# Kernel tuning notes

Hardware: AMD Instinct MI355X
Metric: run time of the kernel (lower is better)

The kernel has to match this reference:

```python
import jax, jax.numpy as jnp
import numpy as np

B, N, M, D, NHEAD, FF, C, K = 2, 16384, 2048, 256, 8, 512, 50, 3
HID = 128          # embed/pos hidden
HEAD_HID = 256     # seg head hidden
L = 4              # depth
EPS = 1e-5


def setup_inputs() -> dict:
    key = jax.random.key(0)
    ks = jax.random.split(key, 32)
    g = lambda i, shape: jax.random.normal(ks[i], shape, dtype=jnp.float32) * 0.02
    z = lambda shape: jnp.zeros(shape, jnp.float32)
    o = lambda shape: jnp.ones(shape, jnp.float32)
    return {
        "xyz": jax.random.normal(ks[0], (B, N, 3), dtype=jnp.float32),
        "embed_w1": g(1, (3, HID)), "embed_b1": z((HID,)),
        "embed_w2": g(2, (HID, D)), "embed_b2": z((D,)),
        "pos_w1": g(3, (3, HID)), "pos_b1": z((HID,)),
        "pos_w2": g(4, (HID, D)), "pos_b2": z((D,)),
        "Wq": g(5, (L, D, D)), "bq": z((L, D)),
        "Wk": g(6, (L, D, D)), "bk": z((L, D)),
        "Wv": g(7, (L, D, D)), "bv": z((L, D)),
        "Wo": g(8, (L, D, D)), "bo": z((L, D)),
        "ln1_s": o((L, D)), "ln1_b": z((L, D)),
        "W1": g(9, (L, D, FF)), "b1": z((L, FF)),
        "W2": g(10, (L, FF, D)), "b2": z((L, D)),
        "ln2_s": o((L, D)), "ln2_b": z((L, D)),
        "head_w1": g(11, (D, HEAD_HID)), "head_b1": z((HEAD_HID,)),
        "head_w2": g(12, (HEAD_HID, C)), "head_b2": z((C,)),
    }


def _ln(x, s, b):
    m = x.mean(-1, keepdims=True)
    v = ((x - m) ** 2).mean(-1, keepdims=True)
    return (x - m) / jnp.sqrt(v + EPS) * s + b


def reference(xyz, embed_w1, embed_b1, embed_w2, embed_b2,
              pos_w1, pos_b1, pos_w2, pos_b2,
              Wq, bq, Wk, bk, Wv, bv, Wo, bo, ln1_s, ln1_b,
              W1, b1, W2, b2, ln2_s, ln2_b,
              head_w1, head_b1, head_w2, head_b2):
    # deterministic token subsample (replaces randperm stub): strided pick of M points
    stride = N // M
    tok = xyz[:, ::stride, :][:, :M]                                  # [B,M,3]
    # per-point embed + learned positional encoding
    x = jax.nn.relu(tok @ embed_w1 + embed_b1) @ embed_w2 + embed_b2  # [B,M,D]
    x = x + jax.nn.relu(tok @ pos_w1 + pos_b1) @ pos_w2 + pos_b2
    dh = D // NHEAD
    scale = 1.0 / jnp.sqrt(jnp.float32(dh))

    def layer(x, p):
        wq, bq_, wk, bk_, wv, bv_, wo, bo_, l1s, l1b, w1, b1_, w2, b2_, l2s, l2b = p
        # pre-norm MHSA
        y = _ln(x, l1s, l1b)
        q = (y @ wq + bq_).reshape(B, M, NHEAD, dh)
        k = (y @ wk + bk_).reshape(B, M, NHEAD, dh)
        v = (y @ wv + bv_).reshape(B, M, NHEAD, dh)
        att = jax.nn.softmax(jnp.einsum('bqhd,bkhd->bhqk', q, k) * scale, axis=-1)
        o = jnp.einsum('bhqk,bkhd->bqhd', att, v).reshape(B, M, D)
        x = x + o @ wo + bo_
        # pre-norm FFN (gelu, exact erf as in torch)
        y = _ln(x, l2s, l2b)
        x = x + jax.nn.gelu(y @ w1 + b1_, approximate=False) @ w2 + b2_
        return x, None

    x, _ = jax.lax.scan(layer, x, (Wq, bq, Wk, bk, Wv, bv, Wo, bo,
                                   ln1_s, ln1_b, W1, b1, W2, b2, ln2_s, ln2_b))
    logits_tok = jax.nn.relu(x @ head_w1 + head_b1) @ head_w2 + head_b2  # [B,M,C]

    # kNN propagation N->M: dist^2 = |q|^2 + |k|^2 - 2 q.k, topk smallest
    q2 = (xyz ** 2).sum(-1)[..., None]            # [B,N,1]
    k2 = (tok ** 2).sum(-1)[:, None, :]           # [B,1,M]
    dist = q2 + k2 - 2.0 * jnp.einsum('bnd,bmd->bnm', xyz, tok)
    dist = jax.lax.stop_gradient(jnp.maximum(dist, 0.0))
    idx = jax.lax.top_k(-dist, K)[1]              # [B,N,K]
    logits_nk = logits_tok[jnp.arange(B)[:, None, None], idx]  # [B,N,K,C]
    return logits_nk.mean(axis=2)                 # [B,N,C]
```

## Files before the change

### kernel.cpp

```cpp
#include <hip/hip_runtime.h>
#include <hip/hip_bf16.h>
#include <math.h>

#define B_ 2
#define N_ 16384
#define M_ 2048
#define D_ 256
#define NHEAD_ 8
#define DH_ 32
#define FF_ 512
#define C_ 50
#define HID_ 128
#define HHID_ 256
#define L_ 4
#define EPS_ 1e-5f
#define TOK_ (B_*M_)
#define QSCALE_ 0.25507604155757994f

typedef short short8 __attribute__((ext_vector_type(8)));
typedef short short4_t __attribute__((ext_vector_type(4)));
typedef float f32x4 __attribute__((ext_vector_type(4)));

__device__ __forceinline__ short f2bf(float f) {
  union { float f; unsigned u; } c; c.f = f;
  unsigned u = c.u;
  unsigned r = (u + 0x7FFFu + ((u >> 16) & 1u)) >> 16;
  return (short)r;
}
__device__ __forceinline__ float fast_exp2(float x) {
  float r;
  asm("v_exp_f32 %0, %1" : "=v"(r) : "v"(x));
  return r;
}
__device__ __forceinline__ unsigned cvt_pk_bf16(float lo, float hi) {
  unsigned r;
  asm("v_cvt_pk_bf16_f32 %0, %1, %2" : "=v"(r) : "v"(lo), "v"(hi));
  return r;
}

__global__ __launch_bounds__(256) void wconv_all(
    const float* __restrict__ Wq, const float* __restrict__ Wk,
    const float* __restrict__ Wv, const float* __restrict__ Wo,
    const float* __restrict__ W1, const float* __restrict__ W2,
    const float* __restrict__ h1,
    short* __restrict__ WqT, short* __restrict__ WkT,
    short* __restrict__ WvT, short* __restrict__ WoT,
    short* __restrict__ W1T, short* __restrict__ W2T, short* __restrict__ h1T) {
  int bid = blockIdx.x;
  const float* W; short* WT; int Kd, Nd, tn, tk;
  if (bid < 256) {
    int mat = bid >> 6, rem = bid & 63, l = rem >> 4, t = rem & 15;
    W  = (mat == 0 ? Wq : mat == 1 ? Wk : mat == 2 ? Wv : Wo) + l * 65536;
    WT = (mat == 0 ? WqT : mat == 1 ? WkT : mat == 2 ? WvT : WoT) + l * 65536;
    Kd = 256; Nd = 256; tn = t & 3; tk = t >> 2;
  } else if (bid < 384) {
    int rem = bid - 256, l = rem >> 5, t = rem & 31;
    W = W1 + l * 131072; WT = W1T + l * 131072;
    Kd = 256; Nd = 512; tn = t & 7; tk = t >> 3;
  } else if (bid < 512) {
    int rem = bid - 384, l = rem >> 5, t = rem & 31;
    W = W2 + l * 131072; WT = W2T + l * 131072;
    Kd = 512; Nd = 256; tn = t & 3; tk = t >> 2;
  } else {
    int t = bid - 512;
    W = h1; WT = h1T; Kd = 256; Nd = 256; tn = t & 3; tk = t >> 2;
  }
  int n0 = tn * 64, k0 = tk * 64;
  __shared__ short ts[64][72];
  int tid = threadIdx.x;
  #pragma unroll
  for (int i = 0; i < 4; ++i) {
    int r = i * 16 + (tid >> 4);
    int c4 = (tid & 15) * 4;
    float4 v = *(const float4*)&W[(size_t)(k0 + r) * Nd + n0 + c4];
    ts[c4 + 0][r] = f2bf(v.x);
    ts[c4 + 1][r] = f2bf(v.y);
    ts[c4 + 2][r] = f2bf(v.z);
    ts[c4 + 3][r] = f2bf(v.w);
  }
  __syncthreads();
  #pragma unroll
  for (int i = 0; i < 2; ++i) {
    int n = i * 32 + (tid >> 3);
    int kc = (tid & 7) * 8;
    *(short8*)&WT[(size_t)(n0 + n) * Kd + k0 + kc] = *(short8*)&ts[n][kc];
  }
}

__global__ __launch_bounds__(128) void embed_kernel(
    const float* __restrict__ xyz,
    const float* __restrict__ ew1, const float* __restrict__ eb1,
    const float* __restrict__ ew2, const float* __restrict__ eb2,
    const float* __restrict__ pw1, const float* __restrict__ pb1,
    const float* __restrict__ pw2, const float* __restrict__ pb2,
    float* __restrict__ x) {
  int t = blockIdx.x;
  int b = t / M_, m = t % M_;
  const float* p = xyz + ((size_t)b * N_ + (size_t)m * 8) * 3;
  float t0 = p[0], t1 = p[1], t2 = p[2];
  __shared__ float he[HID_], hp[HID_];
  int j = threadIdx.x;
  {
    float a = fmaf(t0, ew1[j], fmaf(t1, ew1[HID_ + j], fmaf(t2, ew1[2 * HID_ + j], eb1[j])));
    he[j] = fmaxf(a, 0.f);
    float c = fmaf(t0, pw1[j], fmaf(t1, pw1[HID_ + j], fmaf(t2, pw1[2 * HID_ + j], pb1[j])));
    hp[j] = fmaxf(c, 0.f);
  }
  __syncthreads();
  for (int d = j; d < D_; d += HID_) {
    float acc = eb2[d] + pb2[d];
    for (int k = 0; k < HID_; ++k) {
      acc = fmaf(he[k], ew2[k * D_ + d], acc);
      acc = fmaf(hp[k], pw2[k * D_ + d], acc);
    }
    x[(size_t)t * D_ + d] = acc;
  }
}

__global__ __launch_bounds__(256) void ln_kernel(
    const float* __restrict__ x, const float* __restrict__ s,
    const float* __restrict__ bb, short* __restrict__ y16) {
  int r = blockIdx.x * 4 + (threadIdx.x >> 6);
  int t = threadIdx.x & 63;
  const float4* xr = (const float4*)(x + (size_t)r * D_);
  float4 v = xr[t];
  float sum = v.x + v.y + v.z + v.w;
  #pragma unroll
  for (int o = 1; o < 64; o <<= 1) sum += __shfl_xor(sum, o, 64);
  float mean = sum * (1.f / D_);
  float dx = v.x - mean, dy = v.y - mean, dz = v.z - mean, dw = v.w - mean;
  float vs = dx * dx + dy * dy + dz * dz + dw * dw;
  #pragma unroll
  for (int o = 1; o < 64; o <<= 1) vs += __shfl_xor(vs, o, 64);
  float inv = 1.0f / sqrtf(vs * (1.f / D_) + EPS_);
  float4 sv = ((const float4*)s)[t];
  float4 bv = ((const float4*)bb)[t];
  short4_t ov;
  ov[0] = f2bf(dx * inv * sv.x + bv.x);
  ov[1] = f2bf(dy * inv * sv.y + bv.y);
  ov[2] = f2bf(dz * inv * sv.z + bv.z);
  ov[3] = f2bf(dw * inv * sv.w + bv.w);
  *(short4_t*)(y16 + (size_t)r * D_ + t * 4) = ov;
}

__global__ __launch_bounds__(256) void head2_kernel(
    const float* __restrict__ y, const float* __restrict__ w2,
    const float* __restrict__ b2, float* __restrict__ lt) {
  __shared__ float ys[4][HHID_];
  int w = threadIdx.x >> 6, l = threadIdx.x & 63;
  int t = blockIdx.x * 4 + w;
  float4 v = ((const float4*)(y + (size_t)t * HHID_))[l];
  *(float4*)&ys[w][l * 4] = v;
  int c = l < C_ ? l : 0;
  float a0 = 0.f, a1 = 0.f, a2 = 0.f, a3 = 0.f;
  #pragma unroll 4
  for (int k = 0; k < HHID_; k += 4) {
    a0 = fmaf(ys[w][k + 0], w2[(k + 0) * C_ + c], a0);
    a1 = fmaf(ys[w][k + 1], w2[(k + 1) * C_ + c], a1);
    a2 = fmaf(ys[w][k + 2], w2[(k + 2) * C_ + c], a2);
    a3 = fmaf(ys[w][k + 3], w2[(k + 3) * C_ + c], a3);
  }
  if (l < C_) lt[(size_t)t * C_ + l] = (a0 + a1) + (a2 + a3) + b2[l];
}

template <int ACT, int RES>
__device__ __forceinline__ void gemm16_body(
    const short* __restrict__ A16, const short* __restrict__ WT,
    const float* __restrict__ bias, const float* __restrict__ R,
    float* __restrict__ C, short* __restrict__ C16, float oscale,
    int K, int Ncols, int m0, int n0) {
  __shared__ short As[32][40];
  __shared__ short Bs[64][40];
  int tid = threadIdx.x;
  int w = tid >> 6, l = tid & 63;
  int lq = l & 15, lg = l >> 4;
  int wr = (w & 1) * 16, wc = (w >> 1) * 32;
  int ar = tid >> 3, ak = (tid & 7) * 4;
  int wn = tid & 63, wk = (tid >> 6) * 8;
  f32x4 acc0 = {0.f, 0.f, 0.f, 0.f};
  f32x4 acc1 = {0.f, 0.f, 0.f, 0.f};
  for (int kk = 0; kk < K; kk += 32) {
    __syncthreads();
    *(short4_t*)&As[ar][ak] = *(const short4_t*)&A16[(size_t)(m0 + ar) * K + kk + ak];
    *(short8*)&Bs[wn][wk]   = *(const short8*)&WT[(size_t)(n0 + wn) * K + kk + wk];
    __syncthreads();
    short8 af = *(short8*)&As[wr + lq][lg * 8];
    short8 b0 = *(short8*)&Bs[wc + lq][lg * 8];
    short8 b1 = *(short8*)&Bs[wc + 16 + lq][lg * 8];
    acc0 = __builtin_amdgcn_mfma_f32_16x16x32_bf16(af, b0, acc0, 0, 0, 0);
    acc1 = __builtin_amdgcn_mfma_f32_16x16x32_bf16(af, b1, acc1, 0, 0, 0);
  }
  int row = m0 + wr + lg * 4;
  #pragma unroll
  for (int r = 0; r < 4; ++r) {
    #pragma unroll
    for (int fj = 0; fj < 2; ++fj) {
      int col = n0 + wc + fj * 16 + lq;
      float v = (fj ? acc1[r] : acc0[r]) + bias[col];
      if (ACT == 1) v = fmaxf(v, 0.f);
      else if (ACT == 2) v = 0.5f * v * (1.f + erff(v * 0.70710678118654752f));
      if (RES) v += R[(size_t)(row + r) * Ncols + col];
      if (C)   C[(size_t)(row + r) * Ncols + col] = v;
      if (C16) C16[(size_t)(row + r) * Ncols + col] = f2bf(v * oscale);
    }
  }
}

template <int ACT, int RES>
__global__ __launch_bounds__(256) void gemm16(
    const short* __restrict__ A16, const short* __restrict__ WT,
    const float* __restrict__ bias, const float* __restrict__ R,
    float* __restrict__ C, short* __restrict__ C16,
    int K, int Ncols) {
  gemm16_body<ACT, RES>(A16, WT, bias, R, C, C16, 1.f, K, Ncols,
                        blockIdx.y * 32, blockIdx.x * 64);
}

__global__ __launch_bounds__(256) void qkv16(
    const short* __restrict__ A16,
    const short* __restrict__ WqT, const short* __restrict__ WkT, const short* __restrict__ WvT,
    const float* __restrict__ bq, const float* __restrict__ bk, const float* __restrict__ bv,
    short* __restrict__ q16, short* __restrict__ k16, short* __restrict__ v16) {
  int sel = blockIdx.x >> 2;
  int n0 = (blockIdx.x & 3) << 6;
  const short* WT = sel == 0 ? WqT : (sel == 1 ? WkT : WvT);
  const float* bb = sel == 0 ? bq : (sel == 1 ? bk : bv);
  short* out16 = sel == 0 ? q16 : (sel == 1 ? k16 : v16);
  float oscale = sel == 0 ? QSCALE_ : 1.f;
  gemm16_body<0, 0>(A16, WT, bb, nullptr, nullptr, out16, oscale, D_, D_,
                    blockIdx.y * 32, n0);
}

__global__ __launch_bounds__(256) void vtrans_kernel(
    const short* __restrict__ v16, short* __restrict__ vt16) {
  int bid = blockIdx.x;
  int mt = bid & 31;
  int h = (bid >> 5) & 7;
  int b = bid >> 8;
  __shared__ short ts[64][40];
  int m0 = mt * 64;
  int tid = threadIdx.x;
  int mm = tid >> 2, dd = (tid & 3) * 8;
  *(short8*)&ts[mm][dd] =
      *(const short8*)&v16[(size_t)(b * M_ + m0 + mm) * D_ + h * DH_ + dd];
  __syncthreads();
  int d = tid >> 3, mc = (tid & 7) * 8;
  short8 r;
  #pragma unroll
  for (int j = 0; j < 8; ++j) r[j] = ts[mc + j][d];
  *(short8*)&vt16[(size_t)((b * NHEAD_ + h) * DH_ + d) * M_ + m0 + mc] = r;
}

#define KSTR 40
#define VSTR 72
#define PSTR 72
__global__ __launch_bounds__(256) void attn_mfma_kernel(
    const short* __restrict__ q16, const short* __restrict__ k16,
    const short* __restrict__ vt16,
    float* __restrict__ po0, float* __restrict__ po1,
    float* __restrict__ po2, float* __restrict__ po3,
    float* __restrict__ pl) {
  __shared__ short Ks[64][KSTR];
  __shared__ short Vt[32][VSTR];
  __shared__ short Ps[4][16][PSTR];
  int bid = blockIdx.x;
  int quar = bid & 3;
  int qt = (bid >> 2) & 31;
  int h  = (bid >> 7) & 7;
  int b  = bid >> 10;
  int tid = threadIdx.x;
  int w  = tid >> 6;
  int l  = tid & 63;
  int lq = l & 15;
  int lg = l >> 4;

  short8 qf = *(const short8*)&q16[(size_t)(b * M_ + qt * 64 + w * 16 + lq) * D_ + h * DH_ + lg * 8];

  float l_i = 0.f;
  f32x4 o0 = {0.f, 0.f, 0.f, 0.f};
  f32x4 o1 = {0.f, 0.f, 0.f, 0.f};
  int srow = tid >> 2, scol = (tid & 3) * 8;
  int vd = tid >> 3, vm = (tid & 7) * 8;
  const short* kp = k16 + (size_t)(b * M_ + quar * 512 + srow) * D_ + h * DH_ + scol;
  const short* vp = vt16 + (size_t)((b * NHEAD_ + h) * DH_ + vd) * M_ + quar * 512 + vm;

  for (int kt = 0; kt < 8; ++kt) {
    __syncthreads();
    *(short8*)&Ks[srow][scol] = *(const short8*)(kp + (size_t)(kt * 64) * D_);
    *(short8*)&Vt[vd][vm]     = *(const short8*)(vp + kt * 64);
    __syncthreads();
    f32x4 st[4];
    #pragma unroll
    for (int t = 0; t < 4; ++t) {
      short8 kf = *(short8*)&Ks[t * 16 + lq][lg * 8];
      f32x4 z = {0.f, 0.f, 0.f, 0.f};
      st[t] = __builtin_amdgcn_mfma_f32_16x16x32_bf16(kf, qf, z, 0, 0, 0);
    }
    #pragma unroll
    for (int t = 0; t < 4; ++t)
      #pragma unroll
      for (int r2 = 0; r2 < 4; ++r2) {
        st[t][r2] = fast_exp2(st[t][r2]);
        l_i += st[t][r2];
      }
    {
      unsigned* pw = (unsigned*)&Ps[w][lq][0];
      #pragma unroll
      for (int t = 0; t < 4; ++t) {
        uint2 pk;
        pk.x = cvt_pk_bf16(st[t][0], st[t][1]);
        pk.y = cvt_pk_bf16(st[t][2], st[t][3]);
        *(uint2*)(pw + t * 8 + lg * 2) = pk;
      }
    }
    #pragma unroll
    for (int c = 0; c < 2; ++c) {
      short8 pf = *(short8*)&Ps[w][lq][c * 32 + lg * 8];
      short8 v0 = *(short8*)&Vt[lq][c * 32 + lg * 8];
      short8 v1 = *(short8*)&Vt[16 + lq][c * 32 + lg * 8];
      o0 = __builtin_amdgcn_mfma_f32_16x16x32_bf16(v0, pf, o0, 0, 0, 0);
      o1 = __builtin_amdgcn_mfma_f32_16x16x32_bf16(v1, pf, o1, 0, 0, 0);
    }
  }
  l_i += __shfl_xor(l_i, 16, 64);
  l_i += __shfl_xor(l_i, 32, 64);
  int f = (b * NHEAD_ + h) * M_ + qt * 64 + w * 16 + lq;
  float* pp = (quar == 0 ? po0 : quar == 1 ? po1 : quar == 2 ? po2 : po3) + (size_t)f * 32;
  #pragma unroll
  for (int r2 = 0; r2 < 4; ++r2) pp[lg * 4 + r2] = o0[r2];
  #pragma unroll
  for (int r2 = 0; r2 < 4; ++r2) pp[16 + lg * 4 + r2] = o1[r2];
  if (lg == 0) pl[quar * (16 * M_) + f] = l_i;
}

__global__ __launch_bounds__(256) void attn_combine(
    const float* __restrict__ po0, const float* __restrict__ po1,
    const float* __restrict__ po2, const float* __restrict__ po3,
    const float* __restrict__ pl, short* __restrict__ ob16) {
  int idx = blockIdx.x * 256 + threadIdx.x;
  int f = idx >> 3, dq = (idx & 7) * 4;
  float inv = 1.f / (pl[f] + pl[16 * M_ + f] + pl[32 * M_ + f] + pl[48 * M_ + f]);
  const float4 a = *(const float4*)&po0[(size_t)f * 32 + dq];
  const float4 c = *(const float4*)&po1[(size_t)f * 32 + dq];
  const float4 e = *(const float4*)&po2[(size_t)f * 32 + dq];
  const float4 g = *(const float4*)&po3[(size_t)f * 32 + dq];
  int b = f >> 14, h = (f >> 11) & 7, m = f & (M_ - 1);
  short4_t r;
  r[0] = f2bf((a.x + c.x + e.x + g.x) * inv);
  r[1] = f2bf((a.y + c.y + e.y + g.y) * inv);
  r[2] = f2bf((a.z + c.z + e.z + g.z) * inv);
  r[3] = f2bf((a.w + c.w + e.w + g.w) * inv);
  *(short4_t*)&ob16[(size_t)(b * M_ + m) * D_ + h * DH_ + dq] = r;
}

__global__ __launch_bounds__(512) void knn_kernel(
    const float* __restrict__ xyz, const float* __restrict__ lt,
    float* __restrict__ out) {
  __shared__ float4 tok[2064];
  int b = blockIdx.x >> 8;
  int q0 = (blockIdx.x & 255) << 6;
  int tid = threadIdx.x;
  for (int i = tid; i < M_; i += 512) {
    const float* tp = xyz + ((size_t)b * N_ + (size_t)i * 8) * 3;
    float a = tp[0], bb = tp[1], cc = tp[2];
    tok[i + (i >> 7)] = make_float4(a, bb, cc, a * a + bb * bb + cc * cc);
  }
  __syncthreads();
  int g = tid >> 4, sl = tid & 15;
  int na = q0 + g, nb = q0 + 32 + g;
  const float* qpa = xyz + ((size_t)b * N_ + na) * 3;
  const float* qpb = xyz + ((size_t)b * N_ + nb) * 3;
  float qxa = qpa[0], qya = qpa[1], qza = qpa[2];
  float qxb = qpb[0], qyb = qpb[1], qzb = qpb[2];
  float q2a = qxa * qxa + qya * qya + qza * qza;
  float q2b = qxb * qxb + qyb * qyb + qzb * qzb;
  float a0 = INFINITY, a1 = INFINITY, a2 = INFINITY;
  int ia0 = 0, ia1 = 0, ia2 = 0;
  float e0 = INFINITY, e1 = INFINITY, e2 = INFINITY;
  int ie0 = 0, ie1 = 0, ie2 = 0;
  const float4* cp = &tok[sl * 129];
  int mb0 = sl << 7;
  #pragma unroll 2
  for (int j = 0; j < 128; ++j) {
    float4 t = cp[j];
    float dota = fmaf(qxa, t.x, fmaf(qya, t.y, qza * t.z));
    float da = fmaxf(q2a + t.w - 2.f * dota, 0.f);
    float dotb = fmaf(qxb, t.x, fmaf(qyb, t.y, qzb * t.z));
    float db = fmaxf(q2b + t.w - 2.f * dotb, 0.f);
    if (da < a2) {
      bool c0 = da < a0, c1 = da < a1;
      int m = mb0 + j;
      a2 = c1 ? a1 : da;  ia2 = c1 ? ia1 : m;
      float n1 = c1 ? da : a1; int nj1 = c1 ? m : ia1;
      a1 = c0 ? a0 : n1;  ia1 = c0 ? ia0 : nj1;
      a0 = c0 ? da : a0;  ia0 = c0 ? m : ia0;
    }
    if (db < e2) {
      bool c0 = db < e0, c1 = db < e1;
      int m = mb0 + j;
      e2 = c1 ? e1 : db;  ie2 = c1 ? ie1 : m;
      float n1 = c1 ? db : e1; int nj1 = c1 ? m : ie1;
      e1 = c0 ? e0 : n1;  ie1 = c0 ? ie0 : nj1;
      e0 = c0 ? db : e0;  ie0 = c0 ? m : ie0;
    }
  }
  auto insA = [&](float d, int i) {
    if (d < a2 || (d == a2 && i < ia2)) {
      if (d < a1 || (d == a1 && i < ia1)) {
        a2 = a1; ia2 = ia1;
        if (d < a0 || (d == a0 && i < ia0)) { a1 = a0; ia1 = ia0; a0 = d; ia0 = i; }
        else { a1 = d; ia1 = i; }
      } else { a2 = d; ia2 = i; }
    }
  };
  auto insB = [&](float d, int i) {
    if (d < e2 || (d == e2 && i < ie2)) {
      if (d < e1 || (d == e1 && i < ie1)) {
        e2 = e1; ie2 = ie1;
        if (d < e0 || (d == e0 && i < ie0)) { e1 = e0; ie1 = ie0; e0 = d; ie0 = i; }
        else { e1 = d; ie1 = i; }
      } else { e2 = d; ie2 = i; }
    }
  };
  #pragma unroll
  for (int off = 1; off < 16; off <<= 1) {
    float p0 = __shfl_xor(a0, off, 64); int pi0 = __shfl_xor(ia0, off, 64);
    float p1 = __shfl_xor(a1, off, 64); int pi1 = __shfl_xor(ia1, off, 64);
    float p2 = __shfl_xor(a2, off, 64); int pi2 = __shfl_xor(ia2, off, 64);
    insA(p0, pi0); insA(p1, pi1); insA(p2, pi2);
    float r0 = __shfl_xor(e0, off, 64); int ri0 = __shfl_xor(ie0, off, 64);
    float r1 = __shfl_xor(e1, off, 64); int ri1 = __shfl_xor(ie1, off, 64);
    float r2 = __shfl_xor(e2, off, 64); int ri2 = __shfl_xor(ie2, off, 64);
    insB(r0, ri0); insB(r1, ri1); insB(r2, ri2);
  }
  {
    const float* l0 = lt + ((size_t)b * M_ + ia0) * C_;
    const float* l1 = lt + ((size_t)b * M_ + ia1) * C_;
    const float* l2 = lt + ((size_t)b * M_ + ia2) * C_;
    float* op = out + ((size_t)b * N_ + na) * C_;
    for (int cc = sl; cc < C_; cc += 16)
      op[cc] = (l0[cc] + l1[cc] + l2[cc]) * (1.f / 3.f);
  }
  {
    const float* l0 = lt + ((size_t)b * M_ + ie0) * C_;
    const float* l1 = lt + ((size_t)b * M_ + ie1) * C_;
    const float* l2 = lt + ((size_t)b * M_ + ie2) * C_;
    float* op = out + ((size_t)b * N_ + nb) * C_;
    for (int cc = sl; cc < C_; cc += 16)
      op[cc] = (l0[cc] + l1[cc] + l2[cc]) * (1.f / 3.f);
  }
}

extern "C" void kernel_launch(void* const* d_in, const int* in_sizes, int n_in,
                              void* d_out, int out_size, void* d_ws, size_t ws_size,
                              hipStream_t stream) {
  const float* xyz  = (const float*)d_in[0];
  const float* ew1  = (const float*)d_in[1];
  const float* eb1  = (const float*)d_in[2];
  const float* ew2  = (const float*)d_in[3];
  const float* eb2  = (const float*)d_in[4];
  const float* pw1  = (const float*)d_in[5];
  const float* pb1  = (const float*)d_in[6];
  const float* pw2  = (const float*)d_in[7];
  const float* pb2  = (const float*)d_in[8];
  const float* Wq   = (const float*)d_in[9];
  const float* bq   = (const float*)d_in[10];
  const float* Wk   = (const float*)d_in[11];
  const float* bk   = (const float*)d_in[12];
  const float* Wv   = (const float*)d_in[13];
  const float* bv   = (const float*)d_in[14];
  const float* Wo   = (const float*)d_in[15];
  const float* bo   = (const float*)d_in[16];
  const float* ln1s = (const float*)d_in[17];
  const float* ln1b = (const float*)d_in[18];
  const float* W1   = (const float*)d_in[19];
  const float* b1   = (const float*)d_in[20];
  const float* W2   = (const float*)d_in[21];
  const float* b2   = (const float*)d_in[22];
  const float* ln2s = (const float*)d_in[23];
  const float* ln2b = (const float*)d_in[24];
  const float* hw1  = (const float*)d_in[25];
  const float* hb1  = (const float*)d_in[26];
  const float* hw2  = (const float*)d_in[27];
  const float* hb2  = (const float*)d_in[28];
  float* out = (float*)d_out;

  float* x   = (float*)d_ws;
  float* y   = x + 1048576;
  float* po2 = y + 1048576;
  float* po3 = po2 + 1048576;
  float* lt  = po3 + 1048576;
  short* y16 = (short*)(lt + 204800);
  short* q16 = y16 + 1048576;
  short* k16 = q16 + 1048576;
  short* v16 = k16 + 1048576;
  short* vt16 = v16 + 1048576;
  short* ob16 = vt16 + 1048576;
  short* x16  = ob16 + 1048576;
  short* ff16 = x16 + 1048576;
  short* WqT = ff16 + 2097152;
  short* WkT = WqT + 262144;
  short* WvT = WkT + 262144;
  short* WoT = WvT + 262144;
  short* W1T = WoT + 262144;
  short* W2T = W1T + 524288;
  short* h1T = W2T + 524288;
  float* po0 = y;
  float* po1 = (float*)ff16;
  float* pl  = lt;

  wconv_all<<<528, 256, 0, stream>>>(Wq, Wk, Wv, Wo, W1, W2, hw1,
                                     WqT, WkT, WvT, WoT, W1T, W2T, h1T);
  embed_kernel<<<TOK_, 128, 0, stream>>>(xyz, ew1, eb1, ew2, eb2, pw1, pb1, pw2, pb2, x);

  dim3 gQKV(12, TOK_ / 32);
  dim3 gD(D_ / 64, TOK_ / 32);
  dim3 gF(FF_ / 64, TOK_ / 32);
  for (int l = 0; l < L_; ++l) {
    ln_kernel<<<TOK_ / 4, 256, 0, stream>>>(x, ln1s + l * D_, ln1b + l * D_, y16);
    qkv16<<<gQKV, 256, 0, stream>>>(y16, WqT + l * 65536, WkT + l * 65536, WvT + l * 65536,
                                    bq + l * D_, bk + l * D_, bv + l * D_, q16, k16, v16);
    vtrans_kernel<<<512, 256, 0, stream>>>(v16, vt16);
    attn_mfma_kernel<<<2048, 256, 0, stream>>>(q16, k16, vt16, po0, po1, po2, po3, pl);
    attn_combine<<<1024, 256, 0, stream>>>(po0, po1, po2, po3, pl, ob16);
    gemm16<0, 1><<<gD, 256, 0, stream>>>(ob16, WoT + l * 65536, bo + l * D_, x, x, nullptr, D_, D_);
    ln_kernel<<<TOK_ / 4, 256, 0, stream>>>(x, ln2s + l * D_, ln2b + l * D_, y16);
    gemm16<2, 0><<<gF, 256, 0, stream>>>(y16, W1T + l * 131072, b1 + l * FF_, nullptr, nullptr, ff16, D_, FF_);
    gemm16<0, 1><<<gD, 256, 0, stream>>>(ff16, W2T + l * 131072, b2 + l * D_, x, x, x16, FF_, D_);
  }
  gemm16<1, 0><<<gD, 256, 0, stream>>>(x16, h1T, hb1, nullptr, y, nullptr, D_, HHID_);
  head2_kernel<<<TOK_ / 4, 256, 0, stream>>>(y, hw2, hb2, lt);
  knn_kernel<<<512, 512, 0, stream>>>(xyz, lt, out);
}
```

Baseline: 411.1 us.

## Enlarge GEMM row tile to 64 and split kNN to one query per group

The bf16 MFMA GEMM tile grows from 32x64 to 64x64. Each wave now computes a 2x2 set of 16x16 fragments, which reuses B fragments and halves the B-tile reloads per output row. Separately, the kNN kernel handles one query per 16-lane group instead of two and launches twice as many blocks. That raises parallelism but duplicates the shared-memory token load per block and drops the interleaving of two queries in one thread. The GEMM change halves the GEMM grid size, which may lower occupancy on a large GPU.

```diff
diff --git a/kernel.cpp b/kernel.cpp
--- a/kernel.cpp
+++ b/kernel.cpp
@@ -169,39 +169,47 @@
     const float* __restrict__ bias, const float* __restrict__ R,
     float* __restrict__ C, short* __restrict__ C16, float oscale,
     int K, int Ncols, int m0, int n0) {
-  __shared__ short As[32][40];
+  __shared__ short As[64][40];
   __shared__ short Bs[64][40];
   int tid = threadIdx.x;
   int w = tid >> 6, l = tid & 63;
   int lq = l & 15, lg = l >> 4;
-  int wr = (w & 1) * 16, wc = (w >> 1) * 32;
-  int ar = tid >> 3, ak = (tid & 7) * 4;
-  int wn = tid & 63, wk = (tid >> 6) * 8;
-  f32x4 acc0 = {0.f, 0.f, 0.f, 0.f};
-  f32x4 acc1 = {0.f, 0.f, 0.f, 0.f};
+  int wr = (w & 1) * 32, wc = (w >> 1) * 32;
+  int sr = tid >> 2, sk = (tid & 3) * 8;
+  f32x4 acc00 = {0.f, 0.f, 0.f, 0.f};
+  f32x4 acc01 = {0.f, 0.f, 0.f, 0.f};
+  f32x4 acc10 = {0.f, 0.f, 0.f, 0.f};
+  f32x4 acc11 = {0.f, 0.f, 0.f, 0.f};
   for (int kk = 0; kk < K; kk += 32) {
     __syncthreads();
-    *(short4_t*)&As[ar][ak] = *(const short4_t*)&A16[(size_t)(m0 + ar) * K + kk + ak];
-    *(short8*)&Bs[wn][wk]   = *(const short8*)&WT[(size_t)(n0 + wn) * K + kk + wk];
+    *(short8*)&As[sr][sk] = *(const short8*)&A16[(size_t)(m0 + sr) * K + kk + sk];
+    *(short8*)&Bs[sr][sk] = *(const short8*)&WT[(size_t)(n0 + sr) * K + kk + sk];
     __syncthreads();
-    short8 af = *(short8*)&As[wr + lq][lg * 8];
+    short8 a0 = *(short8*)&As[wr + lq][lg * 8];
+    short8 a1 = *(short8*)&As[wr + 16 + lq][lg * 8];
     short8 b0 = *(short8*)&Bs[wc + lq][lg * 8];
     short8 b1 = *(short8*)&Bs[wc + 16 + lq][lg * 8];
-    acc0 = __builtin_amdgcn_mfma_f32_16x16x32_bf16(af, b0, acc0, 0, 0, 0);
-    acc1 = __builtin_amdgcn_mfma_f32_16x16x32_bf16(af, b1, acc1, 0, 0, 0);
-  }
-  int row = m0 + wr + lg * 4;
-  #pragma unroll
-  for (int r = 0; r < 4; ++r) {
+    acc00 = __builtin_amdgcn_mfma_f32_16x16x32_bf16(a0, b0, acc00, 0, 0, 0);
+    acc01 = __builtin_amdgcn_mfma_f32_16x16x32_bf16(a0, b1, acc01, 0, 0, 0);
+    acc10 = __builtin_amdgcn_mfma_f32_16x16x32_bf16(a1, b0, acc10, 0, 0, 0);
+    acc11 = __builtin_amdgcn_mfma_f32_16x16x32_bf16(a1, b1, acc11, 0, 0, 0);
+  }
+  #pragma unroll
+  for (int fi = 0; fi < 2; ++fi) {
+    int row = m0 + wr + fi * 16 + lg * 4;
     #pragma unroll
-    for (int fj = 0; fj < 2; ++fj) {
-      int col = n0 + wc + fj * 16 + lq;
-      float v = (fj ? acc1[r] : acc0[r]) + bias[col];
-      if (ACT == 1) v = fmaxf(v, 0.f);
-      else if (ACT == 2) v = 0.5f * v * (1.f + erff(v * 0.70710678118654752f));
-      if (RES) v += R[(size_t)(row + r) * Ncols + col];
-      if (C)   C[(size_t)(row + r) * Ncols + col] = v;
-      if (C16) C16[(size_t)(row + r) * Ncols + col] = f2bf(v * oscale);
+    for (int r = 0; r < 4; ++r) {
+      #pragma unroll
+      for (int fj = 0; fj < 2; ++fj) {
+        int col = n0 + wc + fj * 16 + lq;
+        float v = (fi == 0 ? (fj == 0 ? acc00[r] : acc01[r])
+                           : (fj == 0 ? acc10[r] : acc11[r])) + bias[col];
+        if (ACT == 1) v = fmaxf(v, 0.f);
+        else if (ACT == 2) v = 0.5f * v * (1.f + erff(v * 0.70710678118654752f));
+        if (RES) v += R[(size_t)(row + r) * Ncols + col];
+        if (C)   C[(size_t)(row + r) * Ncols + col] = v;
+        if (C16) C16[(size_t)(row + r) * Ncols + col] = f2bf(v * oscale);
+      }
     }
   }
 }
@@ -213,7 +221,7 @@
     float* __restrict__ C, short* __restrict__ C16,
     int K, int Ncols) {
   gemm16_body<ACT, RES>(A16, WT, bias, R, C, C16, 1.f, K, Ncols,
-                        blockIdx.y * 32, blockIdx.x * 64);
+                        blockIdx.y * 64, blockIdx.x * 64);
 }
 
 __global__ __launch_bounds__(256) void qkv16(
@@ -228,7 +236,7 @@
   short* out16 = sel == 0 ? q16 : (sel == 1 ? k16 : v16);
   float oscale = sel == 0 ? QSCALE_ : 1.f;
   gemm16_body<0, 0>(A16, WT, bb, nullptr, nullptr, out16, oscale, D_, D_,
-                    blockIdx.y * 32, n0);
+                    blockIdx.y * 64, n0);
 }
 
 __global__ __launch_bounds__(256) void vtrans_kernel(
@@ -357,8 +365,8 @@
     const float* __restrict__ xyz, const float* __restrict__ lt,
     float* __restrict__ out) {
   __shared__ float4 tok[2064];
-  int b = blockIdx.x >> 8;
-  int q0 = (blockIdx.x & 255) << 6;
+  int b = blockIdx.x >> 9;
+  int q0 = (blockIdx.x & 511) << 5;
   int tid = threadIdx.x;
   for (int i = tid; i < M_; i += 512) {
     const float* tp = xyz + ((size_t)b * N_ + (size_t)i * 8) * 3;
@@ -367,88 +375,50 @@
   }
   __syncthreads();
   int g = tid >> 4, sl = tid & 15;
-  int na = q0 + g, nb = q0 + 32 + g;
-  const float* qpa = xyz + ((size_t)b * N_ + na) * 3;
-  const float* qpb = xyz + ((size_t)b * N_ + nb) * 3;
-  float qxa = qpa[0], qya = qpa[1], qza = qpa[2];
-  float qxb = qpb[0], qyb = qpb[1], qzb = qpb[2];
-  float q2a = qxa * qxa + qya * qya + qza * qza;
-  float q2b = qxb * qxb + qyb * qyb + qzb * qzb;
-  float a0 = INFINITY, a1 = INFINITY, a2 = INFINITY;
-  int ia0 = 0, ia1 = 0, ia2 = 0;
-  float e0 = INFINITY, e1 = INFINITY, e2 = INFINITY;
-  int ie0 = 0, ie1 = 0, ie2 = 0;
+  int n = q0 + g;
+  const float* qp = xyz + ((size_t)b * N_ + n) * 3;
+  float qx = qp[0], qy = qp[1], qz = qp[2];
+  float q2 = qx * qx + qy * qy + qz * qz;
+  float dd0 = INFINITY, dd1 = INFINITY, dd2 = INFINITY;
+  int ii0 = 0, ii1 = 0, ii2 = 0;
   const float4* cp = &tok[sl * 129];
-  int mb0 = sl << 7;
+  int mb = sl << 7;
   #pragma unroll 2
   for (int j = 0; j < 128; ++j) {
     float4 t = cp[j];
-    float dota = fmaf(qxa, t.x, fmaf(qya, t.y, qza * t.z));
-    float da = fmaxf(q2a + t.w - 2.f * dota, 0.f);
-    float dotb = fmaf(qxb, t.x, fmaf(qyb, t.y, qzb * t.z));
-    float db = fmaxf(q2b + t.w - 2.f * dotb, 0.f);
-    if (da < a2) {
-      bool c0 = da < a0, c1 = da < a1;
-      int m = mb0 + j;
-      a2 = c1 ? a1 : da;  ia2 = c1 ? ia1 : m;
-      float n1 = c1 ? da : a1; int nj1 = c1 ? m : ia1;
-      a1 = c0 ? a0 : n1;  ia1 = c0 ? ia0 : nj1;
-      a0 = c0 ? da : a0;  ia0 = c0 ? m : ia0;
-    }
-    if (db < e2) {
-      bool c0 = db < e0, c1 = db < e1;
-      int m = mb0 + j;
-      e2 = c1 ? e1 : db;  ie2 = c1 ? ie1 : m;
-      float n1 = c1 ? db : e1; int nj1 = c1 ? m : ie1;
-      e1 = c0 ? e0 : n1;  ie1 = c0 ? ie0 : nj1;
-      e0 = c0 ? db : e0;  ie0 = c0 ? m : ie0;
-    }
-  }
-  auto insA = [&](float d, int i) {
-    if (d < a2 || (d == a2 && i < ia2)) {
-      if (d < a1 || (d == a1 && i < ia1)) {
-        a2 = a1; ia2 = ia1;
-        if (d < a0 || (d == a0 && i < ia0)) { a1 = a0; ia1 = ia0; a0 = d; ia0 = i; }
-        else { a1 = d; ia1 = i; }
-      } else { a2 = d; ia2 = i; }
+    float dot = fmaf(qx, t.x, fmaf(qy, t.y, qz * t.z));
+    float d = fmaxf(q2 + t.w - 2.f * dot, 0.f);
+    if (d < dd2) {
+      int m = mb + j;
+      if (d < dd1) {
+        dd2 = dd1; ii2 = ii1;
+        if (d < dd0) { dd1 = dd0; ii1 = ii0; dd0 = d; ii0 = m; }
+        else         { dd1 = d;  ii1 = m; }
+      } else         { dd2 = d;  ii2 = m; }
+    }
+  }
+  auto insT = [&](float d, int i) {
+    if (d < dd2 || (d == dd2 && i < ii2)) {
+      if (d < dd1 || (d == dd1 && i < ii1)) {
+        dd2 = dd1; ii2 = ii1;
+        if (d < dd0 || (d == dd0 && i < ii0)) { dd1 = dd0; ii1 = ii0; dd0 = d; ii0 = i; }
+        else { dd1 = d; ii1 = i; }
+      } else { dd2 = d; ii2 = i; }
     }
   };
-  auto insB = [&](float d, int i) {
-    if (d < e2 || (d == e2 && i < ie2)) {
-      if (d < e1 || (d == e1 && i < ie1)) {
-        e2 = e1; ie2 = ie1;
-        if (d < e0 || (d == e0 && i < ie0)) { e1 = e0; ie1 = ie0; e0 = d; ie0 = i; }
-        else { e1 = d; ie1 = i; }
-      } else { e2 = d; ie2 = i; }
-    }
-  };
   #pragma unroll
   for (int off = 1; off < 16; off <<= 1) {
-    float p0 = __shfl_xor(a0, off, 64); int pi0 = __shfl_xor(ia0, off, 64);
-    float p1 = __shfl_xor(a1, off, 64); int pi1 = __shfl_xor(ia1, off, 64);
-    float p2 = __shfl_xor(a2, off, 64); int pi2 = __shfl_xor(ia2, off, 64);
-    insA(p0, pi0); insA(p1, pi1); insA(p2, pi2);
-    float r0 = __shfl_xor(e0, off, 64); int ri0 = __shfl_xor(ie0, off, 64);
-    float r1 = __shfl_xor(e1, off, 64); int ri1 = __shfl_xor(ie1, off, 64);
-    float r2 = __shfl_xor(e2, off, 64); int ri2 = __shfl_xor(ie2, off, 64);
-    insB(r0, ri0); insB(r1, ri1); insB(r2, ri2);
-  }
-  {
-    const float* l0 = lt + ((size_t)b * M_ + ia0) * C_;
-    const float* l1 = lt + ((size_t)b * M_ + ia1) * C_;
-    const float* l2 = lt + ((size_t)b * M_ + ia2) * C_;
-    float* op = out + ((size_t)b * N_ + na) * C_;
-    for (int cc = sl; cc < C_; cc += 16)
-      op[cc] = (l0[cc] + l1[cc] + l2[cc]) * (1.f / 3.f);
-  }
-  {
-    const float* l0 = lt + ((size_t)b * M_ + ie0) * C_;
-    const float* l1 = lt + ((size_t)b * M_ + ie1) * C_;
-    const float* l2 = lt + ((size_t)b * M_ + ie2) * C_;
-    float* op = out + ((size_t)b * N_ + nb) * C_;
-    for (int cc = sl; cc < C_; cc += 16)
-      op[cc] = (l0[cc] + l1[cc] + l2[cc]) * (1.f / 3.f);
-  }
+    float p0 = __shfl_xor(dd0, off, 64); int pi0 = __shfl_xor(ii0, off, 64);
+    float p1 = __shfl_xor(dd1, off, 64); int pi1 = __shfl_xor(ii1, off, 64);
+    float p2 = __shfl_xor(dd2, off, 64); int pi2 = __shfl_xor(ii2, off, 64);
+    insT(p0, pi0); insT(p1, pi1); insT(p2, pi2);
+  }
+  const float* l0 = lt + ((size_t)b * M_ + ii0) * C_;
+  const float* l1 = lt + ((size_t)b * M_ + ii1) * C_;
+  const float* l2 = lt + ((size_t)b * M_ + ii2) * C_;
+  float* op = out + ((size_t)b * N_ + n) * C_;
+  for (int cc = sl; cc < C_; cc += 16)
+    op[cc] = (l0[cc] + l1[cc] + l2[cc]) * (1.f / 3.f);
 }
 
 extern "C" void kernel_launch(void* const* d_in, const int* in_sizes, int n_in,
@@ -513,9 +483,9 @@
                                      WqT, WkT, WvT, WoT, W1T, W2T, h1T);
   embed_kernel<<<TOK_, 128, 0, stream>>>(xyz, ew1, eb1, ew2, eb2, pw1, pb1, pw2, pb2, x);
 
-  dim3 gQKV(12, TOK_ / 32);
-  dim3 gD(D_ / 64, TOK_ / 32);
-  dim3 gF(FF_ / 64, TOK_ / 32);
+  dim3 gQKV(12, TOK_ / 64);
+  dim3 gD(D_ / 64, TOK_ / 64);
+  dim3 gF(FF_ / 64, TOK_ / 64);
   for (int l = 0; l < L_; ++l) {
     ln_kernel<<<TOK_ / 4, 256, 0, stream>>>(x, ln1s + l * D_, ln1b + l * D_, y16);
     qkv16<<<gQKV, 256, 0, stream>>>(y16, WqT + l * 65536, WkT + l * 65536, WvT + l * 65536,
@@ -530,5 +500,5 @@
   }
   gemm16<1, 0><<<gD, 256, 0, stream>>>(x16, h1T, hb1, nullptr, y, nullptr, D_, HHID_);
   head2_kernel<<<TOK_ / 4, 256, 0, stream>>>(y, hw2, hb2, lt);
-  knn_kernel<<<512, 512, 0, stream>>>(xyz, lt, out);
-}
+  knn_kernel<<<1024, 512, 0, stream>>>(xyz, lt, out);
+}
```

New measurement: 402.5 us. -2.1%, faster.
